# Performance work log

Measured on AMD Instinct MI355X. Metric: run time of the kernel, lower is better.

## Reference

```python
import jax, jax.numpy as jnp
import numpy as np

N_NODES = 100000
N_EDGES = 1000000
D = 128
NEG_SLOPE = 0.01  # F.leaky_relu default


def setup_inputs() -> dict:
    key = jax.random.key(0)
    k1, k2, k3, k4, k5, k6 = jax.random.split(key, 6)
    h_src = jax.random.normal(k1, (N_NODES, D), dtype=jnp.float32)
    h_dst = jax.random.normal(k2, (N_NODES, D), dtype=jnp.float32)
    edge_src = jax.random.randint(k3, (N_EDGES,), 0, N_NODES, dtype=jnp.int32)
    edge_dst = jax.random.randint(k4, (N_EDGES,), 0, N_NODES, dtype=jnp.int32)
    # xavier_normal_ on a (1, D) tensor -> std = sqrt(2/(1+D))
    std = float(np.sqrt(2.0 / (1.0 + D)))
    attn_l = jax.random.normal(k5, (D,), dtype=jnp.float32) * std
    attn_r = jax.random.normal(k6, (D,), dtype=jnp.float32) * std
    bias = jnp.zeros((D,), dtype=jnp.float32)
    return {"h_src": h_src, "h_dst": h_dst, "edge_src": edge_src,
            "edge_dst": edge_dst, "attn_l": attn_l, "attn_r": attn_r,
            "bias": bias}


def reference(h_src, h_dst, edge_src, edge_dst, attn_l, attn_r, bias):
    # Per-node attention projections (dot with attn vectors): [N]
    el = h_src @ attn_l
    er = h_dst @ attn_r
    # Edge scores: gather + add + leaky_relu, [E]
    e = jax.nn.leaky_relu(el[edge_src] + er[edge_dst], negative_slope=NEG_SLOPE)
    # Segment (per-destination) softmax over incoming edges
    m = jax.ops.segment_max(e, edge_dst, num_segments=N_NODES)  # [N]
    a = jnp.exp(e - m[edge_dst])                                # [E]
    s = jax.ops.segment_sum(a, edge_dst, num_segments=N_NODES)  # [N]
    alpha = a / s[edge_dst]                                     # [E]
    # dropout p=0.0 -> identity
    # Weighted message + scatter-sum aggregation: [N, D]
    msg = h_src[edge_src] * alpha[:, None]                      # [E, D]
    h_N = jax.ops.segment_sum(msg, edge_dst, num_segments=N_NODES)
    return h_N + bias
```

## Files before the change

### kernel.cpp

```cpp
#include <hip/hip_runtime.h>
#include <math.h>

#define N_NODES 100000
#define N_EDGES 1000000
#define D 128
#define NEG_SLOPE 0.01f
#define CAP 48
#define FILL_BLOCKS 4096

__device__ __forceinline__ unsigned int f2bf(float f) {
    unsigned int u = __float_as_uint(f);
    return (u + 0x7FFFu + ((u >> 16) & 1u)) >> 16;
}

__global__ void proj_kernel(const float* __restrict__ h_src,
                            const float* __restrict__ h_dst,
                            const float* __restrict__ attn_l,
                            const float* __restrict__ attn_r,
                            float2* __restrict__ elr,
                            uint2* __restrict__ hbf,
                            int* __restrict__ cnt) {
    int tid = blockIdx.x * blockDim.x + threadIdx.x;
    if (tid < N_NODES) cnt[tid] = 0;
    int wave = tid >> 6;
    int lane = threadIdx.x & 63;
    int hl = lane & 31;
    int node = wave * 2 + (lane >> 5);
    if (node >= N_NODES) return;
    float4 vs = ((const float4*)(h_src + (size_t)node * D))[hl];
    float4 vd = ((const float4*)(h_dst + (size_t)node * D))[hl];
    float4 al = ((const float4*)attn_l)[hl];
    float4 ar = ((const float4*)attn_r)[hl];
    uint2 pk = { f2bf(vs.x) | (f2bf(vs.y) << 16),
                 f2bf(vs.z) | (f2bf(vs.w) << 16) };
    hbf[(size_t)node * 32 + hl] = pk;
    float sl = vs.x * al.x + vs.y * al.y + vs.z * al.z + vs.w * al.w;
    float sr = vd.x * ar.x + vd.y * ar.y + vd.z * ar.z + vd.w * ar.w;
    #pragma unroll
    for (int off = 16; off > 0; off >>= 1) {
        sl += __shfl_xor(sl, off, 64);
        sr += __shfl_xor(sr, off, 64);
    }
    if (hl == 0) elr[node] = make_float2(sl, sr);
}

__global__ void fill_kernel(const int* __restrict__ esrc,
                            const int* __restrict__ edst,
                            const float2* __restrict__ elr,
                            int* __restrict__ cnt,
                            int2* __restrict__ csr) {
    const int shard = blockIdx.x & 7;
    const int stride = (FILL_BLOCKS / 8) * 256;
    int tid = (blockIdx.x >> 3) * blockDim.x + threadIdx.x;
    for (int i = tid; i < N_EDGES; i += stride) {
        int d = edst[i];
        if ((d & 7) != shard) continue;
        int s = esrc[i];
        float v = elr[s].x + elr[d].y;
        v = (v > 0.0f) ? v : NEG_SLOPE * v;
        int slot = atomicAdd(&cnt[d], 1);
        if (slot < CAP)
            csr[(size_t)d * CAP + slot] = make_int2(s, __float_as_int(__expf(v)));
    }
}

__global__ void aggregate_kernel(const unsigned int* __restrict__ hbf,
                                 const int* __restrict__ cnt,
                                 const int2* __restrict__ csr,
                                 const float* __restrict__ bias,
                                 float* __restrict__ out) {
    int t = blockIdx.x * blockDim.x + threadIdx.x;
    int node = t >> 6;
    if (node >= N_NODES) return;
    int lane = threadIdx.x & 63;
    int q = lane >> 4, ql = lane & 15;
    int deg = min(cnt[node], CAP);
    float4 b0 = ((const float4*)bias)[ql * 2];
    float4 b1 = ((const float4*)bias)[ql * 2 + 1];
    float4* op = (float4*)(out + (size_t)node * D);
    if (deg == 0) {
        if (q == 0) { op[ql * 2] = b0; op[ql * 2 + 1] = b1; }
        return;
    }
    int2 p = csr[(size_t)node * CAP + min(lane, deg - 1)];
    float acc[8] = {0, 0, 0, 0, 0, 0, 0, 0};
    float sum = 0.0f;
    for (int base = 0; base < deg; base += 4) {
        int e = base + q;
        int   sk = __shfl(p.x, e, 64);
        int   wb = __shfl(p.y, e, 64);
        float wk = (e < deg) ? __int_as_float(wb) : 0.0f;
        uint4 g = ((const uint4*)(hbf + (size_t)sk * 64))[ql];
        acc[0] += wk * __uint_as_float(g.x << 16);
        acc[1] += wk * __uint_as_float(g.x & 0xFFFF0000u);
        acc[2] += wk * __uint_as_float(g.y << 16);
        acc[3] += wk * __uint_as_float(g.y & 0xFFFF0000u);
        acc[4] += wk * __uint_as_float(g.z << 16);
        acc[5] += wk * __uint_as_float(g.z & 0xFFFF0000u);
        acc[6] += wk * __uint_as_float(g.w << 16);
        acc[7] += wk * __uint_as_float(g.w & 0xFFFF0000u);
        sum += wk;
    }
    #pragma unroll
    for (int off = 16; off <= 32; off <<= 1) {
        sum += __shfl_xor(sum, off, 64);
        #pragma unroll
        for (int i = 0; i < 8; ++i) acc[i] += __shfl_xor(acc[i], off, 64);
    }
    if (q == 0) {
        float inv = 1.0f / sum;
        float4 o0 = { acc[0] * inv + b0.x, acc[1] * inv + b0.y,
                      acc[2] * inv + b0.z, acc[3] * inv + b0.w };
        float4 o1 = { acc[4] * inv + b1.x, acc[5] * inv + b1.y,
                      acc[6] * inv + b1.z, acc[7] * inv + b1.w };
        op[ql * 2]     = o0;
        op[ql * 2 + 1] = o1;
    }
}

extern "C" void kernel_launch(void* const* d_in, const int* in_sizes, int n_in,
                              void* d_out, int out_size, void* d_ws, size_t ws_size,
                              hipStream_t stream) {
    const float* h_src  = (const float*)d_in[0];
    const float* h_dst  = (const float*)d_in[1];
    const int*   esrc   = (const int*)d_in[2];
    const int*   edst   = (const int*)d_in[3];
    const float* attn_l = (const float*)d_in[4];
    const float* attn_r = (const float*)d_in[5];
    const float* bias   = (const float*)d_in[6];
    float* out = (float*)d_out;

    uint2*  hbf = (uint2*)d_ws;
    int2*   csr = (int2*)(hbf + (size_t)N_NODES * 32);
    float2* elr = (float2*)(csr + (size_t)N_NODES * CAP);
    int*    cnt = (int*)(elr + N_NODES);

    proj_kernel<<<12500, 256, 0, stream>>>(
        h_src, h_dst, attn_l, attn_r, elr, hbf, cnt);

    fill_kernel<<<FILL_BLOCKS, 256, 0, stream>>>(
        esrc, edst, elr, cnt, csr);

    aggregate_kernel<<<25000, 256, 0, stream>>>(
        (const unsigned int*)hbf, cnt, csr, bias, out);
}
```

Baseline: 262.1 us.

## Move edge score computation into aggregate and shard per-destination counters

The fill kernel now stores only the source index per CSR slot, and the aggregate kernel computes each edge's leaky-relu exp weight from separate el/er arrays. This halves CSR write and read traffic and removes the random elr gathers from the atomic fill pass. Counters are split into eight contiguous shards indexed by d>>3, so each fill shard's atomics stay in a compact region. Edge and destination index loads are marked nontemporal. In exchange the aggregate kernel does an extra random el gather per edge, and the gather loop is now guarded by a branch.

```diff
diff --git a/kernel.cpp b/kernel.cpp
--- a/kernel.cpp
+++ b/kernel.cpp
@@ -7,6 +7,7 @@
 #define NEG_SLOPE 0.01f
 #define CAP 48
 #define FILL_BLOCKS 4096
+#define CNT_STRIDE 12512
 
 __device__ __forceinline__ unsigned int f2bf(float f) {
     unsigned int u = __float_as_uint(f);
@@ -17,11 +18,12 @@
                             const float* __restrict__ h_dst,
                             const float* __restrict__ attn_l,
                             const float* __restrict__ attn_r,
-                            float2* __restrict__ elr,
+                            float* __restrict__ el,
+                            float* __restrict__ er,
                             uint2* __restrict__ hbf,
                             int* __restrict__ cnt) {
     int tid = blockIdx.x * blockDim.x + threadIdx.x;
-    if (tid < N_NODES) cnt[tid] = 0;
+    if (tid < 8 * CNT_STRIDE) cnt[tid] = 0;
     int wave = tid >> 6;
     int lane = threadIdx.x & 63;
     int hl = lane & 31;
@@ -41,32 +43,32 @@
         sl += __shfl_xor(sl, off, 64);
         sr += __shfl_xor(sr, off, 64);
     }
-    if (hl == 0) elr[node] = make_float2(sl, sr);
+    if (hl == 0) { el[node] = sl; er[node] = sr; }
 }
 
 __global__ void fill_kernel(const int* __restrict__ esrc,
                             const int* __restrict__ edst,
-                            const float2* __restrict__ elr,
                             int* __restrict__ cnt,
-                            int2* __restrict__ csr) {
+                            int* __restrict__ csr) {
     const int shard = blockIdx.x & 7;
     const int stride = (FILL_BLOCKS / 8) * 256;
     int tid = (blockIdx.x >> 3) * blockDim.x + threadIdx.x;
+    int* cshard = cnt + shard * CNT_STRIDE;
     for (int i = tid; i < N_EDGES; i += stride) {
-        int d = edst[i];
+        int d = __builtin_nontemporal_load(edst + i);
         if ((d & 7) != shard) continue;
-        int s = esrc[i];
-        float v = elr[s].x + elr[d].y;
-        v = (v > 0.0f) ? v : NEG_SLOPE * v;
-        int slot = atomicAdd(&cnt[d], 1);
+        int s = __builtin_nontemporal_load(esrc + i);
+        int slot = atomicAdd(cshard + (d >> 3), 1);
         if (slot < CAP)
-            csr[(size_t)d * CAP + slot] = make_int2(s, __float_as_int(__expf(v)));
+            csr[(size_t)d * CAP + slot] = s;
     }
 }
 
 __global__ void aggregate_kernel(const unsigned int* __restrict__ hbf,
                                  const int* __restrict__ cnt,
-                                 const int2* __restrict__ csr,
+                                 const int* __restrict__ csr,
+                                 const float* __restrict__ el,
+                                 const float* __restrict__ er,
                                  const float* __restrict__ bias,
                                  float* __restrict__ out) {
     int t = blockIdx.x * blockDim.x + threadIdx.x;
@@ -74,7 +76,7 @@
     if (node >= N_NODES) return;
     int lane = threadIdx.x & 63;
     int q = lane >> 4, ql = lane & 15;
-    int deg = min(cnt[node], CAP);
+    int deg = min(cnt[(node & 7) * CNT_STRIDE + (node >> 3)], CAP);
     float4 b0 = ((const float4*)bias)[ql * 2];
     float4 b1 = ((const float4*)bias)[ql * 2 + 1];
     float4* op = (float4*)(out + (size_t)node * D);
@@ -82,24 +84,28 @@
         if (q == 0) { op[ql * 2] = b0; op[ql * 2 + 1] = b1; }
         return;
     }
-    int2 p = csr[(size_t)node * CAP + min(lane, deg - 1)];
+    int sv = csr[(size_t)node * CAP + min(lane, deg - 1)];
+    float v = el[sv] + er[node];
+    v = (v > 0.0f) ? v : NEG_SLOPE * v;
+    float wv = __expf(v);
     float acc[8] = {0, 0, 0, 0, 0, 0, 0, 0};
     float sum = 0.0f;
     for (int base = 0; base < deg; base += 4) {
         int e = base + q;
-        int   sk = __shfl(p.x, e, 64);
-        int   wb = __shfl(p.y, e, 64);
-        float wk = (e < deg) ? __int_as_float(wb) : 0.0f;
-        uint4 g = ((const uint4*)(hbf + (size_t)sk * 64))[ql];
-        acc[0] += wk * __uint_as_float(g.x << 16);
-        acc[1] += wk * __uint_as_float(g.x & 0xFFFF0000u);
-        acc[2] += wk * __uint_as_float(g.y << 16);
-        acc[3] += wk * __uint_as_float(g.y & 0xFFFF0000u);
-        acc[4] += wk * __uint_as_float(g.z << 16);
-        acc[5] += wk * __uint_as_float(g.z & 0xFFFF0000u);
-        acc[6] += wk * __uint_as_float(g.w << 16);
-        acc[7] += wk * __uint_as_float(g.w & 0xFFFF0000u);
-        sum += wk;
+        int   sk = __shfl(sv, e, 64);
+        float wk = __shfl(wv, e, 64);
+        if (e < deg) {
+            uint4 g = ((const uint4*)(hbf + (size_t)sk * 64))[ql];
+            acc[0] += wk * __uint_as_float(g.x << 16);
+            acc[1] += wk * __uint_as_float(g.x & 0xFFFF0000u);
+            acc[2] += wk * __uint_as_float(g.y << 16);
+            acc[3] += wk * __uint_as_float(g.y & 0xFFFF0000u);
+            acc[4] += wk * __uint_as_float(g.z << 16);
+            acc[5] += wk * __uint_as_float(g.z & 0xFFFF0000u);
+            acc[6] += wk * __uint_as_float(g.w << 16);
+            acc[7] += wk * __uint_as_float(g.w & 0xFFFF0000u);
+            sum += wk;
+        }
     }
     #pragma unroll
     for (int off = 16; off <= 32; off <<= 1) {
@@ -130,17 +136,18 @@
     const float* bias   = (const float*)d_in[6];
     float* out = (float*)d_out;
 
-    uint2*  hbf = (uint2*)d_ws;
-    int2*   csr = (int2*)(hbf + (size_t)N_NODES * 32);
-    float2* elr = (float2*)(csr + (size_t)N_NODES * CAP);
-    int*    cnt = (int*)(elr + N_NODES);
+    uint2* hbf = (uint2*)d_ws;
+    int*   csr = (int*)(hbf + (size_t)N_NODES * 32);
+    float* el  = (float*)(csr + (size_t)N_NODES * CAP);
+    float* er  = el + N_NODES;
+    int*   cnt = (int*)(er + N_NODES);
 
     proj_kernel<<<12500, 256, 0, stream>>>(
-        h_src, h_dst, attn_l, attn_r, elr, hbf, cnt);
+        h_src, h_dst, attn_l, attn_r, el, er, hbf, cnt);
 
     fill_kernel<<<FILL_BLOCKS, 256, 0, stream>>>(
-        esrc, edst, elr, cnt, csr);
+        esrc, edst, cnt, csr);
 
     aggregate_kernel<<<25000, 256, 0, stream>>>(
-        (const unsigned int*)hbf, cnt, csr, bias, out);
+        (const unsigned int*)hbf, cnt, csr, el, er, bias, out);
 }
```

New measurement: 258.3 us. No clear change (-1.4%).
